# Optimization experiments

Measured on AMD Instinct MI355X. Metric: run time of the kernel, lower is better.

Reference implementation:

```python
import jax, jax.numpy as jnp
import numpy as np

EPS = 1e-5


def farthest_point_sample(points, npoint):
    # points: [B, N, 3]; returns idx [B, npoint] (int32)
    B, N, _ = points.shape
    # is_center=True: start from the point farthest from the centroid
    centroid = points.mean(axis=1, keepdims=True)            # [B,1,3]
    d0 = jnp.sum((points - centroid) ** 2, axis=-1)           # [B,N]
    farthest = jnp.argmax(d0, axis=-1)                        # [B]
    distance = jnp.full((B, N), 1e10, dtype=points.dtype)

    def step(carry, _):
        dist, far = carry
        cent = jnp.take_along_axis(points, far[:, None, None], axis=1)  # [B,1,3]
        d = jnp.sum((points - cent) ** 2, axis=-1)                       # [B,N]
        dist = jnp.minimum(dist, d)
        new_far = jnp.argmax(dist, axis=-1)
        return (dist, new_far), far

    (_, _), idx = jax.lax.scan(step, (distance, farthest), None, length=npoint)
    return idx.T  # [B, npoint]


def index_points(x, idx):
    # x: [B, N, C], idx: [B, S] -> [B, S, C]
    return jnp.take_along_axis(x, idx[:, :, None], axis=1)


def setup_inputs() -> dict:
    key = jax.random.key(0)
    k1, k2, k3, k4 = jax.random.split(key, 4)
    B, N, in_dim, out_dim = 8, 16384, 128, 256
    points = jax.random.normal(k1, (B, N, 3), dtype=jnp.float32)
    features = jax.random.normal(k2, (B, N, in_dim), dtype=jnp.float32)
    W = jax.random.normal(k3, (out_dim, in_dim), dtype=jnp.float32) * (1.0 / np.sqrt(in_dim))
    b = jax.random.normal(k4, (out_dim,), dtype=jnp.float32) * 0.01
    return {"points": points, "features": features, "W": W, "b": b, "num_points": 4096}


def reference(points, features, W, b, num_points):
    # conv1x1 on features.transpose(-1,-2): [B,in,N] -> [B,out,N]
    x = jnp.einsum('bnc,oc->bon', features, W) + b[None, :, None]  # [B,out,N]
    # InstanceNorm1d (affine=False): normalize over spatial dim N per (b, channel)
    mu = x.mean(axis=-1, keepdims=True)
    var = x.var(axis=-1, keepdims=True)
    x = (x - mu) * jax.lax.rsqrt(var + EPS)
    x = jax.nn.relu(x)
    feats = x.transpose(0, 2, 1)  # [B,N,out]

    idx = farthest_point_sample(points, num_points)  # [B, num_points]
    sampled_points = index_points(points, idx)
    sampled_features = index_points(feats, idx)
    return sampled_points, sampled_features
```

## Files before the change

kernel.cpp:

```cpp
#include <hip/hip_runtime.h>
#include <math.h>

#define B_      8
#define N_      16384
#define CIN_    128
#define COUT_   256
#define NS_     4096

static __device__ __forceinline__ float sqdist_xla(float px, float py, float pz,
                                                   float cx, float cy, float cz) {
  float dx = __fsub_rn(px, cx);
  float dy = __fsub_rn(py, cy);
  float dz = __fsub_rn(pz, cz);
  return __fmaf_rn(dz, dz, __fmaf_rn(dy, dy, __fmul_rn(dx, dx)));
}

__global__ __launch_bounds__(1024) void k1_fps_gram(
    const float* __restrict__ points, const float* __restrict__ features,
    float* __restrict__ outP, int* __restrict__ idxw,
    float* __restrict__ Gred, float* __restrict__ Sred)
{
  __shared__ __align__(16) char LDSB[131072 + 128];
  const int tid = threadIdx.x;

  if (blockIdx.x < B_) {
    const int b = blockIdx.x;
    const float* __restrict__ P = points + (size_t)b * N_ * 3;
    float2*   __restrict__ sXY  = (float2*)LDSB;
    float*    __restrict__ sv   = (float*)(LDSB + 131072);
    unsigned* __restrict__ cellI= (unsigned*)(LDSB + 131072 + 64);
    float*    __restrict__ cent = (float*)(LDSB + 131072 + 80);
    const int lane = tid & 63;
    const int wid  = tid >> 6;

    float z_[16];
    #pragma unroll
    for (int k = 0; k < 16; ++k) {
      const int n = k * 1024 + tid;
      sXY[n] = make_float2(P[3*n+0], P[3*n+1]);
      z_[k]  = P[3*n+2];
    }
    #pragma unroll
    for (int k = 0; k < 16; ++k) asm volatile("" : "+v"(z_[k]));

    if (tid < 3) {
      const int c = tid;
      float acc = P[c];
      for (int n = 1; n < N_; ++n) acc = __fadd_rn(acc, P[3*n + c]);
      cent[c] = __fmul_rn(acc, 6.103515625e-05f);
    }
    if (tid == 0) { cellI[0] = 0xFFFFFFFFu; cellI[1] = 0xFFFFFFFFu; }
    __syncthreads();

    float dd[16];
    float ccx, ccy, ccz;

    {
      const float cx0 = cent[0], cy0 = cent[1], cz0 = cent[2];
      float tlm = -1.0f;
      #pragma unroll
      for (int k = 0; k < 16; ++k) {
        const int n = k * 1024 + tid;
        const float2 xy = sXY[n];
        const float d = sqdist_xla(xy.x, xy.y, z_[k], cx0, cy0, cz0);
        dd[k] = d;
        tlm = fmaxf(tlm, d);
      }
      float wlm = tlm;
      #pragma unroll
      for (int off = 32; off > 0; off >>= 1) wlm = fmaxf(wlm, __shfl_xor(wlm, off));
      if (lane == 0) sv[wid] = wlm;
      __syncthreads();
      float bv = sv[0];
      #pragma unroll
      for (int w = 1; w < 16; ++w) bv = fmaxf(bv, sv[w]);
      if (tlm == bv) {
        int kb = 0x7FFFFFFF;
        #pragma unroll
        for (int k = 15; k >= 0; --k) kb = (dd[k] == bv) ? k : kb;
        atomicMin(&cellI[0], (unsigned)(kb * 1024 + tid));
      }
      __syncthreads();
      const int far = (int)cellI[0];
      const float2 xy = sXY[far];
      ccx = xy.x; ccy = xy.y; ccz = P[3*(size_t)far + 2];
      if (tid == 0) {
        const size_t ob = (size_t)b * NS_;
        outP[ob*3+0] = ccx; outP[ob*3+1] = ccy; outP[ob*3+2] = ccz;
        idxw[ob] = far;
      }
    }
    #pragma unroll
    for (int k = 0; k < 16; ++k) dd[k] = 1e10f;

    for (int s = 1; s < NS_; ++s) {
      const int par = s & 1;
      float tlm = -1.0f;
      #pragma unroll
      for (int k = 0; k < 16; ++k) {
        const int n = k * 1024 + tid;
        const float2 xy = sXY[n];
        const float d  = sqdist_xla(xy.x, xy.y, z_[k], ccx, ccy, ccz);
        const float nd = fminf(dd[k], d);
        dd[k] = nd;
        tlm = fmaxf(tlm, nd);
      }
      float wlm = tlm;
      #pragma unroll
      for (int off = 32; off > 0; off >>= 1) wlm = fmaxf(wlm, __shfl_xor(wlm, off));
      if (lane == 0) sv[wid] = wlm;
      __syncthreads();
      float bv = sv[0];
      #pragma unroll
      for (int w = 1; w < 16; ++w) bv = fmaxf(bv, sv[w]);
      if (tid == 0) cellI[par ^ 1] = 0xFFFFFFFFu;
      if (tlm == bv) {
        int kb = 0x7FFFFFFF;
        #pragma unroll
        for (int k = 15; k >= 0; --k) kb = (dd[k] == bv) ? k : kb;
        atomicMin(&cellI[par], (unsigned)(kb * 1024 + tid));
      }
      __syncthreads();
      const int far = (int)cellI[par];
      const float2 xy = sXY[far];
      ccx = xy.x; ccy = xy.y; ccz = P[3*(size_t)far + 2];
      if (tid == 0) {
        const size_t ob = (size_t)b * NS_ + s;
        outP[ob*3+0] = ccx; outP[ob*3+1] = ccy; outP[ob*3+2] = ccz;
        idxw[ob] = far;
      }
    }
  } else {
    float* __restrict__ Lf = (float*)LDSB;
    const int b = (int)blockIdx.x - B_;
    float acc[4][4];
    #pragma unroll
    for (int i = 0; i < 4; ++i)
      #pragma unroll
      for (int j = 0; j < 4; ++j) acc[i][j] = 0.f;
    float sacc = 0.f;
    const int ti = tid >> 5;
    const int tj = tid & 31;
    const float* fb = features + (size_t)b * N_ * CIN_;
    for (int t32 = 0; t32 < N_/32; ++t32) {
      const float4 v0 = *(const float4*)(fb + ((size_t)t32 * 32 + ti) * CIN_ + tj * 4);
      __syncthreads();
      *(float4*)&Lf[ti*128 + tj*4] = v0;
      __syncthreads();
      #pragma unroll 4
      for (int r = 0; r < 32; ++r) {
        const float4 a4 = *(const float4*)&Lf[r*128 + ti*4];
        const float4 b4 = *(const float4*)&Lf[r*128 + tj*4];
        const float av[4] = {a4.x, a4.y, a4.z, a4.w};
        const float bw[4] = {b4.x, b4.y, b4.z, b4.w};
        #pragma unroll
        for (int i = 0; i < 4; ++i)
          #pragma unroll
          for (int j = 0; j < 4; ++j) acc[i][j] = fmaf(av[i], bw[j], acc[i][j]);
      }
      if (tid < 128) {
        #pragma unroll 8
        for (int r = 0; r < 32; ++r) sacc += Lf[r*128 + tid];
      }
    }
    float* gp = Gred + (size_t)b * (CIN_*CIN_);
    #pragma unroll
    for (int i = 0; i < 4; ++i)
      #pragma unroll
      for (int j = 0; j < 4; ++j)
        gp[(ti*4+i)*CIN_ + tj*4 + j] = acc[i][j];
    if (tid < 128) Sred[b*CIN_ + tid] = sacc;
  }
}

__global__ __launch_bounds__(128) void k2b_stats(
    const float* __restrict__ Gred, const float* __restrict__ Sred,
    const float* __restrict__ W, const float* __restrict__ bias,
    float* __restrict__ stats)
{
  const int b = blockIdx.x >> 8;
  const int o = blockIdx.x & 255;
  const int tid = threadIdx.x;
  __shared__ float sw[CIN_];
  __shared__ float r1[CIN_], r2[CIN_];
  sw[tid] = W[(size_t)o*CIN_ + tid];
  __syncthreads();
  const float* gr = Gred + (size_t)b*CIN_*CIN_ + (size_t)tid*CIN_;
  float g = 0.f;
  #pragma unroll 8
  for (int j = 0; j < CIN_; ++j) g = fmaf(gr[j], sw[j], g);
  r1[tid] = g * sw[tid];
  r2[tid] = sw[tid] * Sred[b*CIN_ + tid];
  __syncthreads();
  for (int stp = 64; stp > 0; stp >>= 1) {
    if (tid < stp) { r1[tid] += r1[tid+stp]; r2[tid] += r2[tid+stp]; }
    __syncthreads();
  }
  if (tid == 0) {
    const float wGw = r1[0], wS = r2[0], bo = bias[o];
    const float invN = 1.0f / (float)N_;
    const float mu  = wS*invN + bo;
    const float ex2 = (wGw + 2.0f*bo*wS)*invN + bo*bo;
    float var = ex2 - mu*mu;
    var = fmaxf(var, 0.0f);
    const float sc = 1.0f / sqrtf(var + 1e-5f);
    stats[((size_t)(b*COUT_ + o))*2 + 0] = wS*invN;
    stats[((size_t)(b*COUT_ + o))*2 + 1] = sc;
  }
}

__global__ __launch_bounds__(256) void k3_out(
    const float* __restrict__ features, const float* __restrict__ W,
    const int* __restrict__ idxw, const float* __restrict__ stats,
    float* __restrict__ outF)
{
  const int tid = threadIdx.x;
  const int b  = blockIdx.x >> 8;
  const int r  = blockIdx.x & 255;
  const int st = r >> 2, ot = r & 3;
  const int s0 = st * 64, o0 = ot * 64;

  __shared__ float Fs[64][129];
  __shared__ float Wt[64][129];
  __shared__ int   sIdx[64];
  __shared__ float sSub[64], sSc[64];

  if (tid < 64) sIdx[tid] = idxw[b*NS_ + s0 + tid];
  if (tid >= 64 && tid < 128) {
    const int oo = tid - 64;
    sSub[oo] = stats[((size_t)(b*COUT_ + o0 + oo))*2 + 0];
    sSc[oo]  = stats[((size_t)(b*COUT_ + o0 + oo))*2 + 1];
  }
  __syncthreads();
  {
    const int row = tid >> 2;
    const int q   = tid & 3;
    const float* fsrc = features + ((size_t)b*N_ + sIdx[row]) * CIN_;
    const float* wsrc = W + (size_t)(o0 + row) * CIN_;
    #pragma unroll
    for (int v = 0; v < 8; ++v) {
      const int c = q*4 + v*16;
      const float4 fv = *(const float4*)(fsrc + c);
      const float4 wv = *(const float4*)(wsrc + c);
      Fs[row][c+0]=fv.x; Fs[row][c+1]=fv.y; Fs[row][c+2]=fv.z; Fs[row][c+3]=fv.w;
      Wt[row][c+0]=wv.x; Wt[row][c+1]=wv.y; Wt[row][c+2]=wv.z; Wt[row][c+3]=wv.w;
    }
  }
  __syncthreads();

  const int ts = tid >> 4, to = tid & 15;
  float acc[4][4];
  #pragma unroll
  for (int i = 0; i < 4; ++i)
    #pragma unroll
    for (int j = 0; j < 4; ++j) acc[i][j] = 0.f;

  #pragma unroll 4
  for (int k = 0; k < CIN_; ++k) {
    const float a0 = Fs[ts*4+0][k], a1 = Fs[ts*4+1][k], a2 = Fs[ts*4+2][k], a3 = Fs[ts*4+3][k];
    const float w0 = Wt[to*4+0][k], w1 = Wt[to*4+1][k], w2 = Wt[to*4+2][k], w3 = Wt[to*4+3][k];
    acc[0][0]=fmaf(a0,w0,acc[0][0]); acc[0][1]=fmaf(a0,w1,acc[0][1]); acc[0][2]=fmaf(a0,w2,acc[0][2]); acc[0][3]=fmaf(a0,w3,acc[0][3]);
    acc[1][0]=fmaf(a1,w0,acc[1][0]); acc[1][1]=fmaf(a1,w1,acc[1][1]); acc[1][2]=fmaf(a1,w2,acc[1][2]); acc[1][3]=fmaf(a1,w3,acc[1][3]);
    acc[2][0]=fmaf(a2,w0,acc[2][0]); acc[2][1]=fmaf(a2,w1,acc[2][1]); acc[2][2]=fmaf(a2,w2,acc[2][2]); acc[2][3]=fmaf(a2,w3,acc[2][3]);
    acc[3][0]=fmaf(a3,w0,acc[3][0]); acc[3][1]=fmaf(a3,w1,acc[3][1]); acc[3][2]=fmaf(a3,w2,acc[3][2]); acc[3][3]=fmaf(a3,w3,acc[3][3]);
  }

  #pragma unroll
  for (int i = 0; i < 4; ++i) {
    float4 o4;
    o4.x = fmaxf((acc[i][0] - sSub[to*4+0]) * sSc[to*4+0], 0.f);
    o4.y = fmaxf((acc[i][1] - sSub[to*4+1]) * sSc[to*4+1], 0.f);
    o4.z = fmaxf((acc[i][2] - sSub[to*4+2]) * sSc[to*4+2], 0.f);
    o4.w = fmaxf((acc[i][3] - sSub[to*4+3]) * sSc[to*4+3], 0.f);
    *(float4*)&outF[((size_t)b*NS_ + s0 + ts*4 + i)*COUT_ + o0 + to*4] = o4;
  }
}

extern "C" void kernel_launch(void* const* d_in, const int* in_sizes, int n_in,
                              void* d_out, int out_size, void* d_ws, size_t ws_size,
                              hipStream_t stream) {
  (void)in_sizes; (void)n_in; (void)out_size; (void)ws_size;
  const float* points   = (const float*)d_in[0];
  const float* features = (const float*)d_in[1];
  const float* W        = (const float*)d_in[2];
  const float* bias     = (const float*)d_in[3];
  float* out  = (float*)d_out;
  float* outP = out;
  float* outF = out + (size_t)B_*NS_*3;

  char* ws = (char*)d_ws;
  int*   idxw  = (int*)  (ws + 0);
  float* Gred  = (float*)(ws + 131072);
  float* Sred  = (float*)(ws + 655360);
  float* stats = (float*)(ws + 659456);

  k1_fps_gram<<<dim3(B_ + B_),  dim3(1024), 0, stream>>>(points, features, outP, idxw, Gred, Sred);
  k2b_stats  <<<dim3(B_*COUT_), dim3(CIN_), 0, stream>>>(Gred, Sred, W, bias, stats);
  k3_out     <<<dim3(B_*256),   dim3(256),  0, stream>>>(features, W, idxw, stats, outF);
}
```

Measured before the change: 6.560 ms.

## Use DPP wave max, LDS atomicMax reduction, and pack z into argmin key

Replaces the shuffle-based wave max with DPP row/broadcast ops and the per-wave LDS array plus 16-way serial max with a single LDS atomicMax on the float bits. This is valid because distances are non-negative. The winning point's z coordinate is packed into a 64-bit atomicMin key, so the global-memory reload of z for each of the 4096 serial FPS steps goes away. The FPS loop is latency-bound, so this trims shuffle latency and a global load from the critical path. In exchange it adds 64-bit LDS atomics and register selects.

```diff
diff --git a/kernel.cpp b/kernel.cpp
--- a/kernel.cpp
+++ b/kernel.cpp
@@ -6,6 +6,8 @@
 #define CIN_    128
 #define COUT_   256
 #define NS_     4096
+
+typedef unsigned long long u64;
 
 static __device__ __forceinline__ float sqdist_xla(float px, float py, float pz,
                                                    float cx, float cy, float cz) {
@@ -13,6 +15,21 @@
   float dy = __fsub_rn(py, cy);
   float dz = __fsub_rn(pz, cz);
   return __fmaf_rn(dz, dz, __fmaf_rn(dy, dy, __fmul_rn(dx, dx)));
+}
+
+static __device__ __forceinline__ float wave64_max_dpp(float x) {
+  int v = __float_as_int(x);
+  #define DPPSTEP(ctrl, rm, bm) { \
+    const int t = __builtin_amdgcn_update_dpp(0, v, (ctrl), (rm), (bm), false); \
+    v = __float_as_int(fmaxf(__int_as_float(v), __int_as_float(t))); }
+  DPPSTEP(0x111, 0xf, 0xf)
+  DPPSTEP(0x112, 0xf, 0xf)
+  DPPSTEP(0x114, 0xf, 0xe)
+  DPPSTEP(0x118, 0xf, 0xc)
+  DPPSTEP(0x142, 0xa, 0xf)
+  DPPSTEP(0x143, 0xc, 0xf)
+  #undef DPPSTEP
+  return __int_as_float(v);
 }
 
 __global__ __launch_bounds__(1024) void k1_fps_gram(
@@ -26,12 +43,11 @@
   if (blockIdx.x < B_) {
     const int b = blockIdx.x;
     const float* __restrict__ P = points + (size_t)b * N_ * 3;
-    float2*   __restrict__ sXY  = (float2*)LDSB;
-    float*    __restrict__ sv   = (float*)(LDSB + 131072);
-    unsigned* __restrict__ cellI= (unsigned*)(LDSB + 131072 + 64);
-    float*    __restrict__ cent = (float*)(LDSB + 131072 + 80);
+    float2*   __restrict__ sXY   = (float2*)LDSB;
+    u64*      __restrict__ cellI = (u64*)(LDSB + 131072);
+    unsigned* __restrict__ cellV = (unsigned*)(LDSB + 131072 + 16);
+    float*    __restrict__ cent  = (float*)(LDSB + 131072 + 24);
     const int lane = tid & 63;
-    const int wid  = tid >> 6;
 
     float z_[16];
     #pragma unroll
@@ -49,7 +65,10 @@
       for (int n = 1; n < N_; ++n) acc = __fadd_rn(acc, P[3*n + c]);
       cent[c] = __fmul_rn(acc, 6.103515625e-05f);
     }
-    if (tid == 0) { cellI[0] = 0xFFFFFFFFu; cellI[1] = 0xFFFFFFFFu; }
+    if (tid == 0) {
+      cellI[0] = ~0ULL; cellI[1] = ~0ULL;
+      cellV[0] = 0u;    cellV[1] = 0u;
+    }
     __syncthreads();
 
     float dd[16];
@@ -66,24 +85,28 @@
         dd[k] = d;
         tlm = fmaxf(tlm, d);
       }
-      float wlm = tlm;
-      #pragma unroll
-      for (int off = 32; off > 0; off >>= 1) wlm = fmaxf(wlm, __shfl_xor(wlm, off));
-      if (lane == 0) sv[wid] = wlm;
-      __syncthreads();
-      float bv = sv[0];
-      #pragma unroll
-      for (int w = 1; w < 16; ++w) bv = fmaxf(bv, sv[w]);
+      const float wlm = wave64_max_dpp(tlm);
+      if (lane == 63) atomicMax(&cellV[0], (unsigned)__float_as_int(wlm));
+      __syncthreads();
+      const float bv = __int_as_float((int)cellV[0]);
+      if (tid == 0) { cellV[1] = 0u; cellI[1] = ~0ULL; }
       if (tlm == bv) {
         int kb = 0x7FFFFFFF;
         #pragma unroll
         for (int k = 15; k >= 0; --k) kb = (dd[k] == bv) ? k : kb;
-        atomicMin(&cellI[0], (unsigned)(kb * 1024 + tid));
-      }
-      __syncthreads();
-      const int far = (int)cellI[0];
+        float zz = z_[0];
+        #pragma unroll
+        for (int k = 1; k < 16; ++k) zz = (kb == k) ? z_[k] : zz;
+        const u64 key = ((u64)(unsigned)(kb * 1024 + tid) << 32)
+                      | (u64)(unsigned)__float_as_int(zz);
+        atomicMin(&cellI[0], key);
+      }
+      __syncthreads();
+      const u64 cw = cellI[0];
+      const int far = (int)(cw >> 32);
+      ccz = __int_as_float((int)(unsigned)cw);
       const float2 xy = sXY[far];
-      ccx = xy.x; ccy = xy.y; ccz = P[3*(size_t)far + 2];
+      ccx = xy.x; ccy = xy.y;
       if (tid == 0) {
         const size_t ob = (size_t)b * NS_;
         outP[ob*3+0] = ccx; outP[ob*3+1] = ccy; outP[ob*3+2] = ccz;
@@ -105,25 +128,28 @@
         dd[k] = nd;
         tlm = fmaxf(tlm, nd);
       }
-      float wlm = tlm;
-      #pragma unroll
-      for (int off = 32; off > 0; off >>= 1) wlm = fmaxf(wlm, __shfl_xor(wlm, off));
-      if (lane == 0) sv[wid] = wlm;
-      __syncthreads();
-      float bv = sv[0];
-      #pragma unroll
-      for (int w = 1; w < 16; ++w) bv = fmaxf(bv, sv[w]);
-      if (tid == 0) cellI[par ^ 1] = 0xFFFFFFFFu;
+      const float wlm = wave64_max_dpp(tlm);
+      if (lane == 63) atomicMax(&cellV[par], (unsigned)__float_as_int(wlm));
+      __syncthreads();
+      const float bv = __int_as_float((int)cellV[par]);
+      if (tid == 0) { cellV[par ^ 1] = 0u; cellI[par ^ 1] = ~0ULL; }
       if (tlm == bv) {
         int kb = 0x7FFFFFFF;
         #pragma unroll
         for (int k = 15; k >= 0; --k) kb = (dd[k] == bv) ? k : kb;
-        atomicMin(&cellI[par], (unsigned)(kb * 1024 + tid));
-      }
-      __syncthreads();
-      const int far = (int)cellI[par];
+        float zz = z_[0];
+        #pragma unroll
+        for (int k = 1; k < 16; ++k) zz = (kb == k) ? z_[k] : zz;
+        const u64 key = ((u64)(unsigned)(kb * 1024 + tid) << 32)
+                      | (u64)(unsigned)__float_as_int(zz);
+        atomicMin(&cellI[par], key);
+      }
+      __syncthreads();
+      const u64 cw = cellI[par];
+      const int far = (int)(cw >> 32);
+      ccz = __int_as_float((int)(unsigned)cw);
       const float2 xy = sXY[far];
-      ccx = xy.x; ccy = xy.y; ccz = P[3*(size_t)far + 2];
+      ccx = xy.x; ccy = xy.y;
       if (tid == 0) {
         const size_t ob = (size_t)b * NS_ + s;
         outP[ob*3+0] = ccx; outP[ob*3+1] = ccy; outP[ob*3+2] = ccz;
```

Result: faster. 5.915 ms, median of 2 (-9.8%).
